# Optimization experiments

Measured on AMD Instinct MI355X. Metric: run time of the kernel, lower is better.

The kernel has to match this reference:

```python
import jax, jax.numpy as jnp
import numpy as np

B, S, H, NH = 4, 2048, 1024, 16
HS = H // NH  # head size 64


def setup_inputs() -> dict:
    key = jax.random.key(0)
    ks = jax.random.split(key, 12)
    inv = 1.0 / np.sqrt(H)
    d = {
        "query": jax.random.normal(ks[0], (B, S, H), jnp.float32),
        "key": jax.random.normal(ks[1], (B, S, H), jnp.float32),
        "value": jax.random.normal(ks[2], (B, S, H), jnp.float32),
        "causal_mask": jnp.tril(jnp.ones((S, S), dtype=bool)),
        "Wq": jax.random.uniform(ks[3], (H, H), jnp.float32, -inv, inv),
        "bq": jax.random.uniform(ks[4], (H,), jnp.float32, -inv, inv),
        "Wk": jax.random.uniform(ks[5], (H, H), jnp.float32, -inv, inv),
        "bk": jax.random.uniform(ks[6], (H,), jnp.float32, -inv, inv),
        "Wv": jax.random.uniform(ks[7], (H, H), jnp.float32, -inv, inv),
        "bv": jax.random.uniform(ks[8], (H,), jnp.float32, -inv, inv),
        "Wo": jax.random.uniform(ks[9], (H, H), jnp.float32, -inv, inv),
        "bo": jax.random.uniform(ks[10], (H,), jnp.float32, -inv, inv),
    }
    return d


def reference(query, key, value, causal_mask, Wq, bq, Wk, bk, Wv, bv, Wo, bo):
    # Linear projections (torch Linear: x @ W.T + b)
    q = query @ Wq.T + bq
    k = key @ Wk.T + bk
    v = value @ Wv.T + bv
    # [B, NH, S, HS]
    q = q.reshape(B, S, NH, HS).transpose(0, 2, 1, 3)
    k = k.reshape(B, S, NH, HS).transpose(0, 2, 1, 3)
    v = v.reshape(B, S, NH, HS).transpose(0, 2, 1, 3)
    scores = jnp.einsum("bhqd,bhkd->bhqk", q, k) / jnp.sqrt(jnp.float32(HS))
    scores = jnp.where(causal_mask[None, None, :, :], scores, -jnp.inf)
    attn = jax.nn.softmax(scores, axis=-1)
    ctx = jnp.einsum("bhqk,bhkd->bhqd", attn, v)
    ctx = ctx.transpose(0, 2, 1, 3).reshape(B, S, H)
    return ctx @ Wo.T + bo
```

## Files before the change

### kernel.cpp

```cpp
#include <hip/hip_runtime.h>
#include <hip/hip_bf16.h>
#include <math.h>

#define B_  4
#define S_  2048
#define H_  1024
#define NH_ 16
#define HS_ 64

typedef __attribute__((ext_vector_type(8))) short bf16x8;
typedef __attribute__((ext_vector_type(4))) float f32x4;

__device__ __forceinline__ short f2bf(float f) {
    unsigned u = __builtin_bit_cast(unsigned, f);
    u += 0x7FFFu + ((u >> 16) & 1u);
    return (short)(u >> 16);
}

typedef __attribute__((address_space(3))) void lds_void;
typedef const __attribute__((address_space(1))) void g_void;
__device__ __forceinline__ void gl_lds16(const void* g, void* l) {
    __builtin_amdgcn_global_load_lds((g_void*)g, (lds_void*)l, 16, 0, 0);
}


__global__ __launch_bounds__(256) void cvt_all_k(
    const float* __restrict__ a0, const float* __restrict__ a1,
    const float* __restrict__ a2, const float* __restrict__ w0,
    const float* __restrict__ w1, const float* __restrict__ w2,
    const float* __restrict__ w3,
    short* o0, short* o1, short* o2, short* o3, short* o4, short* o5, short* o6)
{
    const int y = blockIdx.y;
    const float* ins[7]  = {a0, a1, a2, w0, w1, w2, w3};
    short*       outs[7] = {o0, o1, o2, o3, o4, o5, o6};
    const int n8 = (y < 3) ? (int)((size_t)B_ * S_ * H_ / 8) : (int)((size_t)H_ * H_ / 8);
    const int i = blockIdx.x * 256 + threadIdx.x;
    if (i >= n8) return;
    const float4* p = (const float4*)ins[y] + (size_t)i * 2;
    float4 a = p[0], b = p[1];
    bf16x8 o;
    o[0] = f2bf(a.x); o[1] = f2bf(a.y); o[2] = f2bf(a.z); o[3] = f2bf(a.w);
    o[4] = f2bf(b.x); o[5] = f2bf(b.y); o[6] = f2bf(b.z); o[7] = f2bf(b.w);
    *(bf16x8*)(outs[y] + (size_t)i * 8) = o;
}

__device__ __forceinline__ void gemm_core(
    const short* __restrict__ A, const short* __restrict__ W,
    int m0, int n0, short* As, short* Ws, f32x4 acc[4][4])
{
    const int tid  = threadIdx.x;
    const int w    = tid >> 6;
    const int lane = tid & 63;
    const int l15  = lane & 15;
    const int q4   = lane >> 4;
    const int wm   = w >> 1;
    const int wn   = w & 1;
    const int K    = 1024;
    const int swz  = l15 & 7;

    const char* Abase = (const char*)A + (size_t)m0 * K * 2;
    const char* Wbase = (const char*)W + (size_t)n0 * K * 2;

    #pragma unroll
    for (int mi = 0; mi < 4; ++mi)
        #pragma unroll
        for (int ni = 0; ni < 4; ++ni)
            acc[mi][ni] = (f32x4){0.f, 0.f, 0.f, 0.f};

    for (int k0 = 0; k0 < K; k0 += 64) {
        __syncthreads();
        #pragma unroll
        for (int t = 0; t < 4; ++t) {
            const int ob  = t * 4096 + w * 1024;
            const int idx = t * 256 + w * 64 + lane;
            const int row = idx >> 3;
            const int sc  = (idx & 7) ^ (row & 7);
            gl_lds16(Abase + (size_t)row * (K * 2) + k0 * 2 + sc * 16, (char*)As + ob);
            gl_lds16(Wbase + (size_t)row * (K * 2) + k0 * 2 + sc * 16, (char*)Ws + ob);
        }
        __syncthreads();

        #pragma unroll
        for (int kh = 0; kh < 2; ++kh) {
            bf16x8 af[4], bf[4];
            #pragma unroll
            for (int mi = 0; mi < 4; ++mi)
                af[mi] = *(const bf16x8*)(As + (wm * 64 + mi * 16 + l15) * 64
                                             + (((kh * 4 + q4) ^ swz) * 8));
            #pragma unroll
            for (int ni = 0; ni < 4; ++ni)
                bf[ni] = *(const bf16x8*)(Ws + (wn * 64 + ni * 16 + l15) * 64
                                             + (((kh * 4 + q4) ^ swz) * 8));
            #pragma unroll
            for (int mi = 0; mi < 4; ++mi)
                #pragma unroll
                for (int ni = 0; ni < 4; ++ni)
                    acc[mi][ni] = __builtin_amdgcn_mfma_f32_16x16x32_bf16(
                        af[mi], bf[ni], acc[mi][ni], 0, 0, 0);
        }
    }
}

__global__ __launch_bounds__(256) void gemm_proj_k(
    const short* __restrict__ Aq, const short* __restrict__ Wqb,
    const float* __restrict__ bq, short* __restrict__ qb,
    const short* __restrict__ Ak, const short* __restrict__ Wkb,
    const float* __restrict__ bk, short* __restrict__ kb,
    const short* __restrict__ Wvb, const short* __restrict__ Av,
    const float* __restrict__ bv, short* __restrict__ vtb)
{
    __shared__ short As[128 * 64];
    __shared__ short Ws[128 * 64];

    const int z = blockIdx.z;
    const short *A, *W; const float* bias; short* out;
    if (z == 0)      { A = Aq;  W = Wqb; bias = bq; out = qb;  }
    else if (z == 1) { A = Ak;  W = Wkb; bias = bk; out = kb;  }
    else             { A = Wvb; W = Av;  bias = bv; out = vtb; }
    const int m0 = (z == 2 ? blockIdx.y : blockIdx.x) * 128;
    const int n0 = (z == 2 ? blockIdx.x : blockIdx.y) * 128;

    f32x4 acc[4][4];
    gemm_core(A, W, m0, n0, As, Ws, acc);

    const int tid  = threadIdx.x;
    const int w    = tid >> 6;
    const int lane = tid & 63;
    const int l15  = lane & 15;
    const int q4   = lane >> 4;
    const int wm   = w >> 1;
    const int wn   = w & 1;

    #pragma unroll
    for (int mi = 0; mi < 4; ++mi) {
        #pragma unroll
        for (int r = 0; r < 4; ++r) {
            const int m = m0 + wm * 64 + mi * 16 + q4 * 4 + r;
            #pragma unroll
            for (int ni = 0; ni < 4; ++ni) {
                const int n = n0 + wn * 64 + ni * 16 + l15;
                const float v = acc[mi][ni][r] + bias[z == 2 ? m : n];
                if (z != 2) {
                    const int b = m >> 11, s = m & (S_ - 1);
                    const int h = n >> 6,  d = n & (HS_ - 1);
                    out[(((size_t)b * NH_ + h) * S_ + s) * HS_ + d] = f2bf(v);
                } else {
                    const int b = n >> 11, s = n & (S_ - 1);
                    const int h = m >> 6,  d = m & (HS_ - 1);
                    out[(((size_t)b * NH_ + h) * HS_ + d) * S_ + s] = f2bf(v);
                }
            }
        }
    }
}

__global__ __launch_bounds__(256) void gemm_out_k(
    const short* __restrict__ A, const short* __restrict__ W,
    const float* __restrict__ bias, float* __restrict__ Cout)
{
    __shared__ short As[128 * 64];
    __shared__ short Ws[128 * 64];
    const int m0 = blockIdx.x * 128;
    const int n0 = blockIdx.y * 128;

    f32x4 acc[4][4];
    gemm_core(A, W, m0, n0, As, Ws, acc);

    const int tid  = threadIdx.x;
    const int w    = tid >> 6;
    const int lane = tid & 63;
    const int l15  = lane & 15;
    const int q4   = lane >> 4;
    const int wm   = w >> 1;
    const int wn   = w & 1;

    #pragma unroll
    for (int mi = 0; mi < 4; ++mi)
        #pragma unroll
        for (int r = 0; r < 4; ++r) {
            const int m = m0 + wm * 64 + mi * 16 + q4 * 4 + r;
            #pragma unroll
            for (int ni = 0; ni < 4; ++ni) {
                const int n = n0 + wn * 64 + ni * 16 + l15;
                Cout[(size_t)m * H_ + n] = acc[mi][ni][r] + bias[n];
            }
        }
}

#define PPAD_ 72

__global__ __launch_bounds__(256) void attn_mfma(
    const short* __restrict__ Q, const short* __restrict__ K,
    const short* __restrict__ VT, short* __restrict__ O)
{
    __shared__ short Ks[64 * 64];
    __shared__ short Vt[64 * 64];
    __shared__ short Pl[4][32 * PPAD_];

    const int tid  = threadIdx.x;
    const int w    = tid >> 6;
    const int lane = tid & 63;
    const int l15  = lane & 15;
    const int q4   = lane >> 4;
    const int swz  = l15 & 7;
    const int bh   = blockIdx.y;
    const size_t base = (size_t)bh * S_ * HS_;
    const int b = bh >> 4;
    const int h = bh & 15;
    const float SC = 0.125f * 1.44269504f;

    #pragma unroll 1
    for (int pass = 0; pass < 2; ++pass) {
        const int qt = pass ? (15 - blockIdx.x) : blockIdx.x;

        bf16x8 aQ[2][2];
        #pragma unroll
        for (int mi = 0; mi < 2; ++mi) {
            const int qrow = qt * 128 + w * 32 + mi * 16 + l15;
            #pragma unroll
            for (int kh = 0; kh < 2; ++kh)
                aQ[mi][kh] = *(const bf16x8*)(Q + base + (size_t)qrow * HS_ + kh * 32 + q4 * 8);
        }

        f32x4 accO[2][4];
        float l_p[2][4];
        #pragma unroll
        for (int mi = 0; mi < 2; ++mi) {
            #pragma unroll
            for (int db = 0; db < 4; ++db) accO[mi][db] = (f32x4){0.f, 0.f, 0.f, 0.f};
            #pragma unroll
            for (int r = 0; r < 4; ++r) l_p[mi][r] = 0.f;
        }

        const int ktmax = 2 * qt + 1;
        for (int kt = 0; kt <= ktmax; ++kt) {
            __syncthreads();
            #pragma unroll
            for (int t = 0; t < 2; ++t) {
                const int ob  = t * 4096 + w * 1024;
                const int idx = t * 256 + w * 64 + lane;
                const int r   = idx >> 3;
                const int sc  = (idx & 7) ^ (r & 7);
                gl_lds16(K + base + (size_t)(kt * 64 + r) * HS_ + sc * 8, (char*)Ks + ob);
                gl_lds16(VT + base + (size_t)r * S_ + kt * 64 + sc * 8, (char*)Vt + ob);
            }
            __syncthreads();

            f32x4 sb[2][4];
            #pragma unroll
            for (int nb = 0; nb < 4; ++nb) {
                const short* krow = &Ks[(nb * 16 + l15) * 64];
                bf16x8 b0 = *(const bf16x8*)(krow + ((q4 ^ swz) * 8));
                bf16x8 b1 = *(const bf16x8*)(krow + (((4 + q4) ^ swz) * 8));
                #pragma unroll
                for (int mi = 0; mi < 2; ++mi) {
                    f32x4 a = (f32x4){0.f, 0.f, 0.f, 0.f};
                    a = __builtin_amdgcn_mfma_f32_16x16x32_bf16(aQ[mi][0], b0, a, 0, 0, 0);
                    a = __builtin_amdgcn_mfma_f32_16x16x32_bf16(aQ[mi][1], b1, a, 0, 0, 0);
                    sb[mi][nb] = a;
                }
            }

            const bool need_mask = (kt >= 2 * qt);
            #pragma unroll
            for (int mi = 0; mi < 2; ++mi) {
                const int qb0 = qt * 128 + w * 32 + mi * 16 + q4 * 4;
                if (need_mask) {
                    #pragma unroll
                    for (int nb = 0; nb < 4; ++nb) {
                        const int kj = kt * 64 + nb * 16 + l15;
                        #pragma unroll
                        for (int r = 0; r < 4; ++r)
                            if (kj > qb0 + r) sb[mi][nb][r] = -INFINITY;
                    }
                }
                short* pw = &Pl[w][0];
                #pragma unroll
                for (int nb = 0; nb < 4; ++nb) {
                    #pragma unroll
                    for (int r = 0; r < 4; ++r) {
                        const float p = exp2f(sb[mi][nb][r] * SC);
                        l_p[mi][r] += p;
                        pw[(mi * 16 + q4 * 4 + r) * PPAD_ + nb * 16 + l15] = f2bf(p);
                    }
                }
            }

            bf16x8 aP[2][2];
            #pragma unroll
            for (int mi = 0; mi < 2; ++mi)
                #pragma unroll
                for (int kh = 0; kh < 2; ++kh)
                    aP[mi][kh] = *(const bf16x8*)(&Pl[w][(mi * 16 + l15) * PPAD_ + kh * 32 + q4 * 8]);
            #pragma unroll
            for (int db = 0; db < 4; ++db) {
                const short* vrow = &Vt[(db * 16 + l15) * 64];
                bf16x8 b0 = *(const bf16x8*)(vrow + ((q4 ^ swz) * 8));
                bf16x8 b1 = *(const bf16x8*)(vrow + (((4 + q4) ^ swz) * 8));
                #pragma unroll
                for (int mi = 0; mi < 2; ++mi) {
                    accO[mi][db] = __builtin_amdgcn_mfma_f32_16x16x32_bf16(aP[mi][0], b0, accO[mi][db], 0, 0, 0);
                    accO[mi][db] = __builtin_amdgcn_mfma_f32_16x16x32_bf16(aP[mi][1], b1, accO[mi][db], 0, 0, 0);
                }
            }
        }

        #pragma unroll
        for (int mi = 0; mi < 2; ++mi) {
            #pragma unroll
            for (int r = 0; r < 4; ++r) {
                float ls = l_p[mi][r];
                ls += __shfl_xor(ls, 1);
                ls += __shfl_xor(ls, 2);
                ls += __shfl_xor(ls, 4);
                ls += __shfl_xor(ls, 8);
                const float inv = 1.f / ls;
                const int orow = qt * 128 + w * 32 + mi * 16 + q4 * 4 + r;
                short* op = O + ((size_t)(b * S_ + orow)) * H_ + h * HS_;
                #pragma unroll
                for (int db = 0; db < 4; ++db)
                    op[db * 16 + l15] = f2bf(accO[mi][db][r] * inv);
            }
        }
        __syncthreads();
    }
}

extern "C" void kernel_launch(void* const* d_in, const int* in_sizes, int n_in,
                              void* d_out, int out_size, void* d_ws, size_t ws_size,
                              hipStream_t stream)
{
    const float* query = (const float*)d_in[0];
    const float* key   = (const float*)d_in[1];
    const float* value = (const float*)d_in[2];
    const float* Wq = (const float*)d_in[4];
    const float* bq = (const float*)d_in[5];
    const float* Wk = (const float*)d_in[6];
    const float* bk = (const float*)d_in[7];
    const float* Wv = (const float*)d_in[8];
    const float* bv = (const float*)d_in[9];
    const float* Wo = (const float*)d_in[10];
    const float* bo = (const float*)d_in[11];
    float* out = (float*)d_out;

    const size_t EA = (size_t)B_ * S_ * H_;
    const size_t EW = (size_t)H_ * H_;

    short* Aq  = (short*)d_ws;
    short* Ak  = Aq  + EA;
    short* Av  = Ak  + EA;
    short* Wqb = Av  + EA;
    short* Wkb = Wqb + EW;
    short* Wvb = Wkb + EW;
    short* Wob = Wvb + EW;
    short* qb  = Wob + EW;
    short* kb  = qb  + EA;
    short* vtb = kb  + EA;
    short* cb  = vtb + EA;

    const int M = B_ * S_;

    cvt_all_k<<<dim3((int)(EA / 8 / 256), 7), 256, 0, stream>>>(
        query, key, value, Wq, Wk, Wv, Wo,
        Aq, Ak, Av, Wqb, Wkb, Wvb, Wob);

    gemm_proj_k<<<dim3(M / 128, H_ / 128, 3), 256, 0, stream>>>(
        Aq, Wqb, bq, qb, Ak, Wkb, bk, kb, Wvb, Av, bv, vtb);

    attn_mfma<<<dim3(S_ / 256, B_ * NH_), 256, 0, stream>>>(qb, kb, vtb, cb);

    gemm_out_k<<<dim3(M / 128, H_ / 128), 256, 0, stream>>>(cb, Wob, bo, out);
}
```

Baseline: 375.8 us.

## Double-buffer K/V tiles in attention and transpose score MFMA for vector P stores

The attention kernel now keeps two LDS slots for K and V^T. It prefetches the next key tile asynchronously while computing the current one, and uses a single barrier per iteration instead of two. The QK^T MFMA operands are swapped so each lane holds one query column. That allows the causal mask to be applied per key, lets each lane write P to LDS as a packed 4-element vector, and replaces the per-row 4-step shuffle reduction of the row sums with a 2-step reduction plus a broadcast. s_setprio hints are placed around the MFMA sections. The cost is double the K/V LDS footprint, which may reduce occupancy.

```diff
diff --git a/kernel.cpp b/kernel.cpp
--- a/kernel.cpp
+++ b/kernel.cpp
@@ -9,6 +9,7 @@
 #define HS_ 64
 
 typedef __attribute__((ext_vector_type(8))) short bf16x8;
+typedef __attribute__((ext_vector_type(4))) short bf16x4;
 typedef __attribute__((ext_vector_type(4))) float f32x4;
 
 __device__ __forceinline__ short f2bf(float f) {
@@ -194,8 +195,8 @@
     const short* __restrict__ Q, const short* __restrict__ K,
     const short* __restrict__ VT, short* __restrict__ O)
 {
-    __shared__ short Ks[64 * 64];
-    __shared__ short Vt[64 * 64];
+    __shared__ short Ks[2][64 * 64];
+    __shared__ short Vt[2][64 * 64];
     __shared__ short Pl[4][32 * PPAD_];
 
     const int tid  = threadIdx.x;
@@ -210,9 +211,27 @@
     const int h = bh & 15;
     const float SC = 0.125f * 1.44269504f;
 
+#define STAGE_KV(slot_, kt_)                                                      \
+    do {                                                                          \
+        _Pragma("unroll")                                                         \
+        for (int t = 0; t < 2; ++t) {                                             \
+            const int ob  = (slot_) * 8192 + t * 4096 + w * 1024;                 \
+            const int idx = t * 256 + w * 64 + lane;        \
+            const int r   = idx >> 3;                                             \
+            const int sc  = (idx & 7) ^ (r & 7);          \
+            gl_lds16(K + base + (size_t)((kt_) * 64 + r) * HS_ + sc * 8,          \
+                     (char*)Ks + ob);                                             \
+            gl_lds16(VT + base + (size_t)r * S_ + (kt_) * 64 + sc * 8,            \
+                     (char*)Vt + ob);                                             \
+        }                                                                         \
+    } while (0)
+
     #pragma unroll 1
     for (int pass = 0; pass < 2; ++pass) {
         const int qt = pass ? (15 - blockIdx.x) : blockIdx.x;
+        const int ktmax = 2 * qt + 1;
+
+        STAGE_KV(0, 0);
 
         bf16x8 aQ[2][2];
         #pragma unroll
@@ -224,66 +243,57 @@
         }
 
         f32x4 accO[2][4];
-        float l_p[2][4];
+        float lsum[2];
         #pragma unroll
         for (int mi = 0; mi < 2; ++mi) {
             #pragma unroll
             for (int db = 0; db < 4; ++db) accO[mi][db] = (f32x4){0.f, 0.f, 0.f, 0.f};
-            #pragma unroll
-            for (int r = 0; r < 4; ++r) l_p[mi][r] = 0.f;
-        }
-
-        const int ktmax = 2 * qt + 1;
+            lsum[mi] = 0.f;
+        }
+
+        __syncthreads();
+
         for (int kt = 0; kt <= ktmax; ++kt) {
-            __syncthreads();
-            #pragma unroll
-            for (int t = 0; t < 2; ++t) {
-                const int ob  = t * 4096 + w * 1024;
-                const int idx = t * 256 + w * 64 + lane;
-                const int r   = idx >> 3;
-                const int sc  = (idx & 7) ^ (r & 7);
-                gl_lds16(K + base + (size_t)(kt * 64 + r) * HS_ + sc * 8, (char*)Ks + ob);
-                gl_lds16(VT + base + (size_t)r * S_ + kt * 64 + sc * 8, (char*)Vt + ob);
-            }
-            __syncthreads();
-
-            f32x4 sb[2][4];
+            const int cur = kt & 1;
+            if (kt < ktmax) STAGE_KV(cur ^ 1, kt + 1);
+
+            f32x4 sbT[2][4];
+            const short* KsBase = &Ks[cur][0];
+            __builtin_amdgcn_s_setprio(1);
             #pragma unroll
             for (int nb = 0; nb < 4; ++nb) {
-                const short* krow = &Ks[(nb * 16 + l15) * 64];
-                bf16x8 b0 = *(const bf16x8*)(krow + ((q4 ^ swz) * 8));
-                bf16x8 b1 = *(const bf16x8*)(krow + (((4 + q4) ^ swz) * 8));
+                const short* krow = KsBase + (nb * 16 + l15) * 64;
+                bf16x8 k0 = *(const bf16x8*)(krow + ((q4 ^ swz) * 8));
+                bf16x8 k1 = *(const bf16x8*)(krow + (((4 + q4) ^ swz) * 8));
                 #pragma unroll
                 for (int mi = 0; mi < 2; ++mi) {
                     f32x4 a = (f32x4){0.f, 0.f, 0.f, 0.f};
-                    a = __builtin_amdgcn_mfma_f32_16x16x32_bf16(aQ[mi][0], b0, a, 0, 0, 0);
-                    a = __builtin_amdgcn_mfma_f32_16x16x32_bf16(aQ[mi][1], b1, a, 0, 0, 0);
-                    sb[mi][nb] = a;
+                    a = __builtin_amdgcn_mfma_f32_16x16x32_bf16(k0, aQ[mi][0], a, 0, 0, 0);
+                    a = __builtin_amdgcn_mfma_f32_16x16x32_bf16(k1, aQ[mi][1], a, 0, 0, 0);
+                    sbT[mi][nb] = a;
                 }
             }
+            __builtin_amdgcn_s_setprio(0);
 
             const bool need_mask = (kt >= 2 * qt);
             #pragma unroll
             for (int mi = 0; mi < 2; ++mi) {
-                const int qb0 = qt * 128 + w * 32 + mi * 16 + q4 * 4;
-                if (need_mask) {
-                    #pragma unroll
-                    for (int nb = 0; nb < 4; ++nb) {
-                        const int kj = kt * 64 + nb * 16 + l15;
-                        #pragma unroll
-                        for (int r = 0; r < 4; ++r)
-                            if (kj > qb0 + r) sb[mi][nb][r] = -INFINITY;
-                    }
-                }
-                short* pw = &Pl[w][0];
+                const int qrow = qt * 128 + w * 32 + mi * 16 + l15;
                 #pragma unroll
                 for (int nb = 0; nb < 4; ++nb) {
+                    bf16x4 pk;
                     #pragma unroll
                     for (int r = 0; r < 4; ++r) {
-                        const float p = exp2f(sb[mi][nb][r] * SC);
-                        l_p[mi][r] += p;
-                        pw[(mi * 16 + q4 * 4 + r) * PPAD_ + nb * 16 + l15] = f2bf(p);
+                        float sv = sbT[mi][nb][r];
+                        if (need_mask) {
+                            const int kj = kt * 64 + nb * 16 + q4 * 4 + r;
+                            if (kj > qrow) sv = -INFINITY;
+                        }
+                        const float p = exp2f(sv * SC);
+                        lsum[mi] += p;
+                        pk[r] = f2bf(p);
                     }
+                    *(bf16x4*)&Pl[w][(mi * 16 + l15) * PPAD_ + nb * 16 + q4 * 4] = pk;
                 }
             }
 
@@ -293,29 +303,32 @@
                 #pragma unroll
                 for (int kh = 0; kh < 2; ++kh)
                     aP[mi][kh] = *(const bf16x8*)(&Pl[w][(mi * 16 + l15) * PPAD_ + kh * 32 + q4 * 8]);
+            const short* VtBase = &Vt[cur][0];
+            __builtin_amdgcn_s_setprio(1);
             #pragma unroll
             for (int db = 0; db < 4; ++db) {
-                const short* vrow = &Vt[(db * 16 + l15) * 64];
-                bf16x8 b0 = *(const bf16x8*)(vrow + ((q4 ^ swz) * 8));
-                bf16x8 b1 = *(const bf16x8*)(vrow + (((4 + q4) ^ swz) * 8));
+                const short* vrow = VtBase + (db * 16 + l15) * 64;
+                bf16x8 v0 = *(const bf16x8*)(vrow + ((q4 ^ swz) * 8));
+                bf16x8 v1 = *(const bf16x8*)(vrow + (((4 + q4) ^ swz) * 8));
                 #pragma unroll
                 for (int mi = 0; mi < 2; ++mi) {
-                    accO[mi][db] = __builtin_amdgcn_mfma_f32_16x16x32_bf16(aP[mi][0], b0, accO[mi][db], 0, 0, 0);
-                    accO[mi][db] = __builtin_amdgcn_mfma_f32_16x16x32_bf16(aP[mi][1], b1, accO[mi][db], 0, 0, 0);
+                    accO[mi][db] = __builtin_amdgcn_mfma_f32_16x16x32_bf16(aP[mi][0], v0, accO[mi][db], 0, 0, 0);
+                    accO[mi][db] = __builtin_amdgcn_mfma_f32_16x16x32_bf16(aP[mi][1], v1, accO[mi][db], 0, 0, 0);
                 }
             }
+            __builtin_amdgcn_s_setprio(0);
+
+            __syncthreads();
         }
 
         #pragma unroll
         for (int mi = 0; mi < 2; ++mi) {
+            float ls = lsum[mi];
+            ls += __shfl_xor(ls, 16);
+            ls += __shfl_xor(ls, 32);
             #pragma unroll
             for (int r = 0; r < 4; ++r) {
-                float ls = l_p[mi][r];
-                ls += __shfl_xor(ls, 1);
-                ls += __shfl_xor(ls, 2);
-                ls += __shfl_xor(ls, 4);
-                ls += __shfl_xor(ls, 8);
-                const float inv = 1.f / ls;
+                const float inv = 1.f / __shfl(ls, q4 * 4 + r);
                 const int orow = qt * 128 + w * 32 + mi * 16 + q4 * 4 + r;
                 short* op = O + ((size_t)(b * S_ + orow)) * H_ + h * HS_;
                 #pragma unroll
@@ -323,8 +336,8 @@
                     op[db * 16 + l15] = f2bf(accO[mi][db][r] * inv);
             }
         }
-        __syncthreads();
     }
+#undef STAGE_KV
 }
 
 extern "C" void kernel_launch(void* const* d_in, const int* in_sizes, int n_in,
```

Result: no change. 380.6 us (+1.3%).
